# Optimization experiments

Measured on AMD Instinct MI355X. Metric: run time of the kernel, lower is better.

## Reference

```python
import jax, jax.numpy as jnp
import numpy as np

B, N, NP, K, C_IN, C, H = 16, 4096, 1024, 32, 128, 256, 4
C_G = C_IN + 3  # grouped feature dim (use_xyz concat of relative coords)
EPS = 1e-3      # keras LayerNormalization default epsilon


def setup_inputs() -> dict:
    key = jax.random.key(0)
    ks = jax.random.split(key, 16)
    s = 0.05
    return {
        "xyz": jax.random.normal(ks[0], (B, N, 3), jnp.float32),
        "newxyz": jax.random.normal(ks[1], (B, NP, 3), jnp.float32),
        "feature_input": jax.random.normal(ks[2], (B, N, C_IN), jnp.float32),
        "w_qkv": jax.random.normal(ks[3], (C_G, 3 * C), jnp.float32) * s,
        "proj_w": jax.random.normal(ks[4], (C, C), jnp.float32) * s,
        "proj_b": jnp.zeros((C,), jnp.float32),
        "dense_w": jax.random.normal(ks[5], (C_G, C), jnp.float32) * s,
        "dense_b": jnp.zeros((C,), jnp.float32),
        "fc1_w": jax.random.normal(ks[6], (C, 2 * C), jnp.float32) * s,
        "fc1_b": jnp.zeros((2 * C,), jnp.float32),
        "fc2_w": jax.random.normal(ks[7], (2 * C, C), jnp.float32) * s,
        "fc2_b": jnp.zeros((C,), jnp.float32),
        "n1_g": jnp.ones((C_G,), jnp.float32),
        "n1_b": jnp.zeros((C_G,), jnp.float32),
        "n2_g": jnp.ones((C,), jnp.float32),
        "n2_b": jnp.zeros((C,), jnp.float32),
        "group_num": K,
        "training": True,
    }


def _layernorm(x, g, b):
    m = jnp.mean(x, axis=-1, keepdims=True)
    v = jnp.mean(jnp.square(x - m), axis=-1, keepdims=True)
    return (x - m) * jax.lax.rsqrt(v + EPS) * g + b


def _sample_and_group(newxyz, group_num, xyz, feats):
    # squared pairwise distances (B, NP, N)
    d2 = (jnp.sum(newxyz**2, -1)[:, :, None]
          - 2.0 * jnp.einsum('bpc,bnc->bpn', newxyz, xyz)
          + jnp.sum(xyz**2, -1)[:, None, :])
    _, idx = jax.lax.top_k(-d2, group_num)            # (B, NP, K) nearest
    b_idx = jnp.arange(newxyz.shape[0])[:, None, None]
    grouped_xyz = xyz[b_idx, idx] - newxyz[:, :, None, :]   # (B, NP, K, 3)
    grouped_feat = feats[b_idx, idx]                        # (B, NP, K, C_IN)
    return jnp.concatenate([grouped_xyz, grouped_feat], axis=-1)


def _self_attention(x, w_qkv, proj_w, proj_b):
    b, n, k = x.shape[0], x.shape[1], x.shape[2]
    d = C // H
    qkv = jnp.einsum('bnkc,cd->bnkd', x, w_qkv)
    qkv = qkv.reshape(b, n, k, 3, H, d)
    qkv = jnp.transpose(qkv, (3, 0, 1, 4, 2, 5))      # (3, B, NP, H, K, d)
    q, kk, v = qkv[0], qkv[1], qkv[2]
    qm = jnp.max(q, axis=-2, keepdims=True)           # (B, NP, H, 1, d)
    attn = jnp.einsum('bnhqd,bnhkd->bnhqk', qm, kk) * (C ** -0.5)
    attn = jax.nn.softmax(attn, axis=-1)
    out = jnp.einsum('bnhqk,bnhkd->bnhqd', attn, v)[..., 0, :]  # (B, NP, H, d)
    out = out.reshape(b, n, C)
    return jax.nn.relu(out @ proj_w + proj_b)


def reference(xyz, newxyz, feature_input, w_qkv, proj_w, proj_b, dense_w,
              dense_b, fc1_w, fc1_b, fc2_w, fc2_b, n1_g, n1_b, n2_g, n2_b,
              group_num, training):
    gf = _sample_and_group(newxyz, group_num, xyz, feature_input)  # (B,NP,K,C_G)
    feat = _self_attention(_layernorm(gf, n1_g, n1_b), w_qkv, proj_w, proj_b)
    feat = feat + jax.nn.relu(jnp.max(gf, axis=-2) @ dense_w + dense_b)
    f2 = _layernorm(feat, n2_g, n2_b)
    f2 = jax.nn.relu(f2 @ fc1_w + fc1_b)
    f2 = f2 @ fc2_w + fc2_b
    return f2 + feat
```

## Files before the change

### kernel.cpp

```cpp
#include <hip/hip_runtime.h>
#include <hip/hip_bf16.h>

typedef __hip_bfloat16 bf16;

#define Bn   16
#define Nn   4096
#define NPn  1024
#define Kn   32
#define CINn 128
#define CGn  131
#define Cn   256
#define Hn   4
#define KPAD 160
#define XBS  168
#define XFS2 136
#define GFS  136

typedef __attribute__((ext_vector_type(8))) short frag_ab;
typedef __attribute__((ext_vector_type(4))) float frag_cd;

__device__ __forceinline__ float b2f(bf16 x) { return __bfloat162float(x); }
__device__ __forceinline__ bf16  f2b(float x) { return __float2bfloat16(x); }
__device__ __forceinline__ short f2bs(float x) {
  union { bf16 h; short s; } u; u.h = __float2bfloat16(x); return u.s;
}
__device__ __forceinline__ float bs2f(short s) {
  union { short v; bf16 h; } u; u.v = s; return __bfloat162float(u.h);
}
__device__ __forceinline__ unsigned f2ord(float f) {
  unsigned u = __float_as_uint(f);
  return u ^ ((u >> 31) ? 0xffffffffu : 0x80000000u);
}

__global__ __launch_bounds__(256) void knn_kernel(const float* __restrict__ xyz,
                                                  const float* __restrict__ newxyz,
                                                  int* __restrict__ idx_out) {
  constexpr int CAP = 2048;
  __shared__ unsigned long long tmin[256];
  __shared__ __align__(16) unsigned long long cand[CAP + 4];
  __shared__ unsigned long long wtau[4];
  __shared__ unsigned long long wred[4];
  __shared__ int scnt;
  const int bp  = blockIdx.x;
  const int b   = bp >> 10;
  const int tid = threadIdx.x;
  const float qx = newxyz[bp*3 + 0];
  const float qy = newxyz[bp*3 + 1];
  const float qz = newxyz[bp*3 + 2];
  const float sn = __fadd_rn(__fadd_rn(__fmul_rn(qx,qx), __fmul_rn(qy,qy)),
                             __fmul_rn(qz,qz));
  const float* xb = xyz + (size_t)b * Nn * 3;
  unsigned long long key[16];
  unsigned long long lmin = ~0ull;
  #pragma unroll
  for (int s = 0; s < 16; ++s) {
    const int n = s*256 + tid;
    const float xx = xb[n*3 + 0];
    const float xy = xb[n*3 + 1];
    const float xz = xb[n*3 + 2];
    const float sx  = __fadd_rn(__fadd_rn(__fmul_rn(xx,xx), __fmul_rn(xy,xy)),
                                __fmul_rn(xz,xz));
    const float dot = __fadd_rn(__fadd_rn(__fmul_rn(qx,xx), __fmul_rn(qy,xy)),
                                __fmul_rn(qz,xz));
    const float d2 = __fadd_rn(__fsub_rn(sn, __fmul_rn(2.0f, dot)), sx);
    key[s] = ((unsigned long long)f2ord(d2) << 32) | (unsigned)n;
    if (key[s] < lmin) lmin = key[s];
  }
  const int lane = tid & 63, wv = tid >> 6;

  if (tid == 0) scnt = 0;
  tmin[tid] = lmin;
  __syncthreads();

  {
    const unsigned long long* wt = &tmin[wv * 64];
    int rk = 0;
    #pragma unroll 8
    for (int j = 0; j < 64; ++j) rk += (wt[j] < lmin) ? 1 : 0;
    if (rk == 31) wtau[wv] = lmin;
  }
  __syncthreads();
  unsigned long long tau = wtau[0];
  if (wtau[1] < tau) tau = wtau[1];
  if (wtau[2] < tau) tau = wtau[2];
  if (wtau[3] < tau) tau = wtau[3];

  #pragma unroll
  for (int s = 0; s < 16; ++s) {
    if (key[s] <= tau) {
      const int p = atomicAdd(&scnt, 1);
      if (p < CAP) cand[p] = key[s];
    }
  }
  __syncthreads();
  const int m = scnt;

  if (m <= CAP) {
    if (tid < 4) cand[m + tid] = ~0ull;
    __syncthreads();
    const int m4 = (m + 3) & ~3;
    for (int t = tid; t < m; t += 256) {
      const unsigned long long mykey = cand[t];
      int r = 0;
      for (int j = 0; j < m4; j += 4) {
        r += (cand[j+0] < mykey) ? 1 : 0;
        r += (cand[j+1] < mykey) ? 1 : 0;
        r += (cand[j+2] < mykey) ? 1 : 0;
        r += (cand[j+3] < mykey) ? 1 : 0;
      }
      if (r < Kn) idx_out[(size_t)bp*Kn + r] = (int)(mykey & 0xffffffffu);
    }
  } else {
    for (int s = 0; s < Kn; ++s) {
      unsigned long long mm = lmin;
      #pragma unroll
      for (int d = 32; d; d >>= 1) {
        const unsigned lo = __shfl_xor((unsigned)(mm & 0xffffffffu), d, 64);
        const unsigned hi = __shfl_xor((unsigned)(mm >> 32), d, 64);
        const unsigned long long o = ((unsigned long long)hi << 32) | lo;
        if (o < mm) mm = o;
      }
      if (lane == 0) wred[wv] = mm;
      __syncthreads();
      unsigned long long best = wred[0];
      if (wred[1] < best) best = wred[1];
      if (wred[2] < best) best = wred[2];
      if (wred[3] < best) best = wred[3];
      __syncthreads();
      const int n = (int)(best & 0xffffffffu);
      if (tid == 0) idx_out[(size_t)bp*Kn + s] = n;
      if ((n & 255) == tid) {
        const int slot = n >> 8;
        #pragma unroll
        for (int t = 0; t < 16; ++t) if (t == slot) key[t] = ~0ull;
        unsigned long long m2 = ~0ull;
        #pragma unroll
        for (int t = 0; t < 16; ++t) if (key[t] < m2) m2 = key[t];
        lmin = m2;
      }
    }
  }
}

__global__ __launch_bounds__(256) void wprep_all_kernel(
    const float* __restrict__ w_qkv, const float* __restrict__ proj_w,
    const float* __restrict__ dense_w, const float* __restrict__ fc1_w,
    const float* __restrict__ fc2_w, short* __restrict__ o_qkv,
    short* __restrict__ o_proj, short* __restrict__ o_dense,
    short* __restrict__ o_fc1, short* __restrict__ o_fc2) {
  const int blk = blockIdx.x;
  const float* W; short* out; int K, N, nnt, remap, base;
  if      (blk <  480) { W=w_qkv;   out=o_qkv;   K=CGn; N=768; nnt=48; remap=1; base=0;    }
  else if (blk <  736) { W=proj_w;  out=o_proj;  K=Cn;  N=256; nnt=16; remap=0; base=480;  }
  else if (blk <  896) { W=dense_w; out=o_dense; K=CGn; N=256; nnt=16; remap=1; base=736;  }
  else if (blk < 1408) { W=fc1_w;   out=o_fc1;   K=Cn;  N=512; nnt=32; remap=0; base=896;  }
  else                 { W=fc2_w;   out=o_fc2;   K=512; N=256; nnt=16; remap=0; base=1408; }
  const int t = (blk - base) * 256 + threadIdx.x;
  const int j    = t & 7;
  const int lane = (t >> 3) & 63;
  const int nt   = (t >> 9) % nnt;
  const int kt   = (t >> 9) / nnt;
  const int k = kt*32 + (lane >> 4)*8 + j;
  const int n = nt*16 + (lane & 15);
  int krow = k;
  if (remap) krow = (k < 128) ? k + 3 : k - 128;
  out[t] = (k < K) ? f2bs(W[(size_t)krow*N + n]) : (short)0;
}

__global__ __launch_bounds__(256, 2) void fused_attn_kernel(
    const float* __restrict__ xyz, const float* __restrict__ newxyz,
    const float* __restrict__ featin, const short* __restrict__ wfrag,
    const float* __restrict__ n1g, const float* __restrict__ n1b,
    const int* __restrict__ idx, bf16* __restrict__ attnout,
    bf16* __restrict__ gfmax) {
  __shared__ __align__(16) short Xs[64 * XBS];
  __shared__ float sg[CGn], sb[CGn];
  __shared__ int sidx[64];
  const int bp0 = blockIdx.x * 2;
  const int b   = bp0 >> 10;
  const int tid = threadIdx.x;
  if (tid < 64) {
    int n = idx[(size_t)bp0*Kn + tid];
    sidx[tid] = ((unsigned)n < (unsigned)Nn) ? n : 0;
  }
  if (tid < CGn) {
    const int rj = (tid < 128) ? tid + 3 : tid - 128;
    sg[tid] = n1g[rj];
    sb[tid] = n1b[rj];
  }
  __syncthreads();
  const int kk = tid >> 3, sub = tid & 7;
  float4 r[2][4];
  float ex[2] = {0.f, 0.f};
  #pragma unroll
  for (int p = 0; p < 2; ++p) {
    const int row = p*32 + kk;
    const float* frow = featin + ((size_t)b*Nn + sidx[row])*CINn;
    #pragma unroll
    for (int i = 0; i < 4; ++i) r[p][i] = *(const float4*)(frow + sub*4 + 32*i);
    if (sub < 3)
      ex[p] = xyz[((size_t)b*Nn + sidx[row])*3 + sub] - newxyz[(bp0+p)*3 + sub];
  }
  #pragma unroll
  for (int p = 0; p < 2; ++p) {
    const int row = p*32 + kk;
    #pragma unroll
    for (int i = 0; i < 4; ++i) {
      short4 s4 = { f2bs(r[p][i].x), f2bs(r[p][i].y), f2bs(r[p][i].z), f2bs(r[p][i].w) };
      *(short4*)&Xs[row*XFS2 + sub*4 + 32*i] = s4;
    }
    if (sub < 3) Xs[row*XFS2 + 128 + sub] = f2bs(ex[p]);
  }
  float mean[2], rstd[2];
  #pragma unroll
  for (int p = 0; p < 2; ++p) {
    float s = ex[p], s2 = ex[p]*ex[p];
    #pragma unroll
    for (int i = 0; i < 4; ++i) {
      s  += r[p][i].x + r[p][i].y + r[p][i].z + r[p][i].w;
      s2 += r[p][i].x*r[p][i].x + r[p][i].y*r[p][i].y
          + r[p][i].z*r[p][i].z + r[p][i].w*r[p][i].w;
    }
    s  += __shfl_xor(s, 1, 64);  s  += __shfl_xor(s, 2, 64);  s  += __shfl_xor(s, 4, 64);
    s2 += __shfl_xor(s2, 1, 64); s2 += __shfl_xor(s2, 2, 64); s2 += __shfl_xor(s2, 4, 64);
    mean[p] = s * (1.0f/CGn);
    const float var = s2 * (1.0f/CGn) - mean[p]*mean[p];
    rstd[p] = rsqrtf(var + 1e-3f);
  }
  __syncthreads();
  #pragma unroll
  for (int p = 0; p < 2; ++p) {
    if (tid < GFS) {
      float m = 0.f;
      if (tid < CGn) {
        m = -1e30f;
        #pragma unroll
        for (int k2 = 0; k2 < Kn; ++k2)
          m = fmaxf(m, bs2f(Xs[(p*32 + k2)*XFS2 + tid]));
      }
      gfmax[(size_t)(bp0+p)*GFS + tid] = f2b(m);
    }
  }
  __syncthreads();
  #pragma unroll
  for (int p = 0; p < 2; ++p) {
    const int row = p*32 + kk;
    #pragma unroll
    for (int i = 0; i < 4; ++i) {
      const float4 g4 = *(const float4*)&sg[sub*4 + 32*i];
      const float4 b4 = *(const float4*)&sb[sub*4 + 32*i];
      short4 s4;
      s4.x = f2bs((r[p][i].x - mean[p])*rstd[p]*g4.x + b4.x);
      s4.y = f2bs((r[p][i].y - mean[p])*rstd[p]*g4.y + b4.y);
      s4.z = f2bs((r[p][i].z - mean[p])*rstd[p]*g4.z + b4.z);
      s4.w = f2bs((r[p][i].w - mean[p])*rstd[p]*g4.w + b4.w);
      *(short4*)&Xs[row*XBS + sub*4 + 32*i] = s4;
    }
    if (sub < 3)
      Xs[row*XBS + 128 + sub] = f2bs((ex[p] - mean[p])*rstd[p]*sg[128+sub] + sb[128+sub]);
  }
  #pragma unroll
  for (int u = 0; u < 8; ++u) {
    const int e = u*256 + tid;
    const int row = e >> 5, jj = 131 + (e & 31);
    if (jj < 160) Xs[row*XBS + jj] = 0;
  }
  __syncthreads();
  const int lane = tid & 63, w = tid >> 6;
  const int col = lane & 15, quad = lane >> 4;
  float qm[2][4], aw[2][2][4], inv[2];
  {
    frag_cd acc[4][4] = {};
    for (int kt = 0; kt < 5; ++kt) {
      const int ko = kt*32 + quad*8;
      frag_ab a[4];
      #pragma unroll
      for (int mt = 0; mt < 4; ++mt)
        a[mt] = *(const frag_ab*)&Xs[(mt*16 + col)*XBS + ko];
      #pragma unroll
      for (int ntl = 0; ntl < 4; ++ntl) {
        const int nt = w*4 + ntl;
        const frag_ab bfr = *(const frag_ab*)(wfrag + ((size_t)(kt*48 + nt)*64 + lane)*8);
        #pragma unroll
        for (int mt = 0; mt < 4; ++mt)
          acc[ntl][mt] = __builtin_amdgcn_mfma_f32_16x16x32_bf16(a[mt], bfr, acc[ntl][mt], 0, 0, 0);
      }
    }
    #pragma unroll
    for (int p = 0; p < 2; ++p)
      #pragma unroll
      for (int ntl = 0; ntl < 4; ++ntl) {
        float m = -1e30f;
        #pragma unroll
        for (int mtl = 0; mtl < 2; ++mtl)
          #pragma unroll
          for (int rr = 0; rr < 4; ++rr) m = fmaxf(m, acc[ntl][p*2+mtl][rr]);
        m = fmaxf(m, __shfl_xor(m, 16, 64));
        m = fmaxf(m, __shfl_xor(m, 32, 64));
        qm[p][ntl] = m;
      }
  }
  {
    frag_cd acc[4][4] = {};
    for (int kt = 0; kt < 5; ++kt) {
      const int ko = kt*32 + quad*8;
      frag_ab a[4];
      #pragma unroll
      for (int mt = 0; mt < 4; ++mt)
        a[mt] = *(const frag_ab*)&Xs[(mt*16 + col)*XBS + ko];
      #pragma unroll
      for (int ntl = 0; ntl < 4; ++ntl) {
        const int nt = 16 + w*4 + ntl;
        const frag_ab bfr = *(const frag_ab*)(wfrag + ((size_t)(kt*48 + nt)*64 + lane)*8);
        #pragma unroll
        for (int mt = 0; mt < 4; ++mt)
          acc[ntl][mt] = __builtin_amdgcn_mfma_f32_16x16x32_bf16(a[mt], bfr, acc[ntl][mt], 0, 0, 0);
      }
    }
    #pragma unroll
    for (int p = 0; p < 2; ++p) {
      float lg[2][4];
      #pragma unroll
      for (int mtl = 0; mtl < 2; ++mtl)
        #pragma unroll
        for (int rr = 0; rr < 4; ++rr) {
          float pp = 0.f;
          #pragma unroll
          for (int ntl = 0; ntl < 4; ++ntl) pp = fmaf(qm[p][ntl], acc[ntl][p*2+mtl][rr], pp);
          #pragma unroll
          for (int d = 1; d < 16; d <<= 1) pp += __shfl_xor(pp, d, 64);
          lg[mtl][rr] = pp * 0.0625f;
        }
      float mx = -1e30f;
      #pragma unroll
      for (int mtl = 0; mtl < 2; ++mtl)
        #pragma unroll
        for (int rr = 0; rr < 4; ++rr) mx = fmaxf(mx, lg[mtl][rr]);
      mx = fmaxf(mx, __shfl_xor(mx, 16, 64));
      mx = fmaxf(mx, __shfl_xor(mx, 32, 64));
      float ssum = 0.f;
      #pragma unroll
      for (int mtl = 0; mtl < 2; ++mtl)
        #pragma unroll
        for (int rr = 0; rr < 4; ++rr) { aw[p][mtl][rr] = expf(lg[mtl][rr] - mx); ssum += aw[p][mtl][rr]; }
      ssum += __shfl_xor(ssum, 16, 64);
      ssum += __shfl_xor(ssum, 32, 64);
      inv[p] = 1.f / ssum;
    }
  }
  {
    frag_cd acc[4][4] = {};
    for (int kt = 0; kt < 5; ++kt) {
      const int ko = kt*32 + quad*8;
      frag_ab a[4];
      #pragma unroll
      for (int mt = 0; mt < 4; ++mt)
        a[mt] = *(const frag_ab*)&Xs[(mt*16 + col)*XBS + ko];
      #pragma unroll
      for (int ntl = 0; ntl < 4; ++ntl) {
        const int nt = 32 + w*4 + ntl;
        const frag_ab bfr = *(const frag_ab*)(wfrag + ((size_t)(kt*48 + nt)*64 + lane)*8);
        #pragma unroll
        for (int mt = 0; mt < 4; ++mt)
          acc[ntl][mt] = __builtin_amdgcn_mfma_f32_16x16x32_bf16(a[mt], bfr, acc[ntl][mt], 0, 0, 0);
      }
    }
    #pragma unroll
    for (int p = 0; p < 2; ++p)
      #pragma unroll
      for (int ntl = 0; ntl < 4; ++ntl) {
        float o = 0.f;
        #pragma unroll
        for (int mtl = 0; mtl < 2; ++mtl)
          #pragma unroll
          for (int rr = 0; rr < 4; ++rr) o = fmaf(aw[p][mtl][rr], acc[ntl][p*2+mtl][rr], o);
        o += __shfl_xor(o, 16, 64);
        o += __shfl_xor(o, 32, 64);
        if (quad == 0)
          attnout[(size_t)(bp0+p)*Cn + w*64 + ntl*16 + col] = f2b(o * inv[p]);
      }
  }
}

template<bool RELU, bool ADD_S, bool OUT_BF16>
__global__ __launch_bounds__(256) void mfma_gemm_kernel(
    const bf16* __restrict__ A, int lda, int Ka,
    const short* __restrict__ Wf, int nnt_total, int N,
    const float* __restrict__ bias, const bf16* __restrict__ S,
    void* __restrict__ Dv) {
  __shared__ __align__(16) short As[64*40];
  const int m0 = blockIdx.y * 64;
  const int n0 = blockIdx.x * 128;
  const int tid = threadIdx.x, lane = tid & 63, w = tid >> 6;
  const int col = lane & 15, quad = lane >> 4;
  const int row = tid >> 2, c8 = (tid & 3) * 8;
  frag_cd acc[4][2] = {};
  const int nkt = (Ka + 31) >> 5;
  for (int kt = 0; kt < nkt; ++kt) {
    const int k0 = kt*32 + c8;
    frag_ab av = {0,0,0,0,0,0,0,0};
    if (k0 + 8 <= Ka)
      av = *(const frag_ab*)((const short*)A + (size_t)(m0+row)*lda + k0);
    __syncthreads();
    *(frag_ab*)&As[row*40 + c8] = av;
    __syncthreads();
    frag_ab afr[4];
    #pragma unroll
    for (int mt = 0; mt < 4; ++mt)
      afr[mt] = *(const frag_ab*)&As[(mt*16 + col)*40 + quad*8];
    #pragma unroll
    for (int ntl = 0; ntl < 2; ++ntl) {
      const int nt = (n0 >> 4) + w*2 + ntl;
      const frag_ab bfr = *(const frag_ab*)(Wf + ((size_t)(kt*nnt_total + nt)*64 + lane)*8);
      #pragma unroll
      for (int mt = 0; mt < 4; ++mt)
        acc[mt][ntl] = __builtin_amdgcn_mfma_f32_16x16x32_bf16(afr[mt], bfr, acc[mt][ntl], 0, 0, 0);
    }
  }
  #pragma unroll
  for (int ntl = 0; ntl < 2; ++ntl) {
    const int n = n0 + w*32 + ntl*16 + col;
    const float bv = bias[n];
    #pragma unroll
    for (int mt = 0; mt < 4; ++mt) {
      #pragma unroll
      for (int r = 0; r < 4; ++r) {
        const int m = m0 + mt*16 + quad*4 + r;
        float v = acc[mt][ntl][r] + bv;
        if (RELU) v = fmaxf(v, 0.f);
        if (ADD_S) v += b2f(S[(size_t)m*N + n]);
        if (OUT_BF16) ((bf16*)Dv)[(size_t)m*N + n] = f2b(v);
        else          ((float*)Dv)[(size_t)m*N + n] = v;
      }
    }
  }
}

__global__ __launch_bounds__(256) void dual_gemm_kernel(
    const bf16* __restrict__ A1, const short* __restrict__ W1,
    const bf16* __restrict__ A2, const short* __restrict__ W2,
    const float* __restrict__ b1, const float* __restrict__ b2,
    bf16* __restrict__ D) {
  __shared__ __align__(16) short As[64*40];
  const int m0 = blockIdx.y * 64;
  const int n0 = blockIdx.x * 128;
  const int tid = threadIdx.x, lane = tid & 63, w = tid >> 6;
  const int col = lane & 15, quad = lane >> 4;
  const int row = tid >> 2, c8 = (tid & 3) * 8;
  frag_cd acc1[4][2] = {}, acc2[4][2] = {};
  for (int kt = 0; kt < 8; ++kt) {
    const frag_ab av = *(const frag_ab*)((const short*)A1 + (size_t)(m0+row)*Cn + kt*32 + c8);
    __syncthreads();
    *(frag_ab*)&As[row*40 + c8] = av;
    __syncthreads();
    frag_ab afr[4];
    #pragma unroll
    for (int mt = 0; mt < 4; ++mt)
      afr[mt] = *(const frag_ab*)&As[(mt*16 + col)*40 + quad*8];
    #pragma unroll
    for (int ntl = 0; ntl < 2; ++ntl) {
      const int nt = (n0 >> 4) + w*2 + ntl;
      const frag_ab bfr = *(const frag_ab*)(W1 + ((size_t)(kt*16 + nt)*64 + lane)*8);
      #pragma unroll
      for (int mt = 0; mt < 4; ++mt)
        acc1[mt][ntl] = __builtin_amdgcn_mfma_f32_16x16x32_bf16(afr[mt], bfr, acc1[mt][ntl], 0, 0, 0);
    }
  }
  for (int kt = 0; kt < 5; ++kt) {
    const int k0 = kt*32 + c8;
    frag_ab av = {0,0,0,0,0,0,0,0};
    if (k0 + 8 <= GFS)
      av = *(const frag_ab*)((const short*)A2 + (size_t)(m0+row)*GFS + k0);
    __syncthreads();
    *(frag_ab*)&As[row*40 + c8] = av;
    __syncthreads();
    frag_ab afr[4];
    #pragma unroll
    for (int mt = 0; mt < 4; ++mt)
      afr[mt] = *(const frag_ab*)&As[(mt*16 + col)*40 + quad*8];
    #pragma unroll
    for (int ntl = 0; ntl < 2; ++ntl) {
      const int nt = (n0 >> 4) + w*2 + ntl;
      const frag_ab bfr = *(const frag_ab*)(W2 + ((size_t)(kt*16 + nt)*64 + lane)*8);
      #pragma unroll
      for (int mt = 0; mt < 4; ++mt)
        acc2[mt][ntl] = __builtin_amdgcn_mfma_f32_16x16x32_bf16(afr[mt], bfr, acc2[mt][ntl], 0, 0, 0);
    }
  }
  #pragma unroll
  for (int ntl = 0; ntl < 2; ++ntl) {
    const int n = n0 + w*32 + ntl*16 + col;
    const float bv1 = b1[n], bv2 = b2[n];
    #pragma unroll
    for (int mt = 0; mt < 4; ++mt) {
      #pragma unroll
      for (int r = 0; r < 4; ++r) {
        const int m = m0 + mt*16 + quad*4 + r;
        const float v = fmaxf(acc1[mt][ntl][r] + bv1, 0.f)
                      + fmaxf(acc2[mt][ntl][r] + bv2, 0.f);
        D[(size_t)m*Cn + n] = f2b(v);
      }
    }
  }
}

__global__ __launch_bounds__(256) void ln2_kernel(const bf16* __restrict__ feat,
                                                  const float* __restrict__ g,
                                                  const float* __restrict__ b,
                                                  bf16* __restrict__ out) {
  const int r = blockIdx.x*4 + (threadIdx.x >> 6), lane = threadIdx.x & 63;
  float vv[4];
  #pragma unroll
  for (int c = 0; c < 4; ++c) vv[c] = b2f(feat[(size_t)r*Cn + lane*4 + c]);
  float s  = vv[0] + vv[1] + vv[2] + vv[3];
  float s2 = vv[0]*vv[0] + vv[1]*vv[1] + vv[2]*vv[2] + vv[3]*vv[3];
  #pragma unroll
  for (int d = 32; d; d >>= 1) { s += __shfl_xor(s, d, 64); s2 += __shfl_xor(s2, d, 64); }
  const float mean = s * (1.f/256.f);
  const float var  = s2 * (1.f/256.f) - mean*mean;
  const float rstd = rsqrtf(var + 1e-3f);
  #pragma unroll
  for (int c = 0; c < 4; ++c) {
    const int cc = lane*4 + c;
    out[(size_t)r*Cn + cc] = f2b((vv[c] - mean)*rstd*g[cc] + b[cc]);
  }
}

extern "C" void kernel_launch(void* const* d_in, const int* in_sizes, int n_in,
                              void* d_out, int out_size, void* d_ws, size_t ws_size,
                              hipStream_t stream) {
  const float* xyz     = (const float*)d_in[0];
  const float* newxyz  = (const float*)d_in[1];
  const float* featin  = (const float*)d_in[2];
  const float* w_qkv   = (const float*)d_in[3];
  const float* proj_w  = (const float*)d_in[4];
  const float* proj_b  = (const float*)d_in[5];
  const float* dense_w = (const float*)d_in[6];
  const float* dense_b = (const float*)d_in[7];
  const float* fc1_w   = (const float*)d_in[8];
  const float* fc1_b   = (const float*)d_in[9];
  const float* fc2_w   = (const float*)d_in[10];
  const float* fc2_b   = (const float*)d_in[11];
  const float* n1g     = (const float*)d_in[12];
  const float* n1b     = (const float*)d_in[13];
  const float* n2g     = (const float*)d_in[14];
  const float* n2b     = (const float*)d_in[15];

  char*  ws     = (char*)d_ws;
  short* wqkv   = (short*)(ws + 0);
  short* wproj  = (short*)(ws + 245760);
  short* wdense = (short*)(ws + 376832);
  short* wfc1   = (short*)(ws + 458752);
  short* wfc2   = (short*)(ws + 720896);
  bf16*  featB  = (bf16*)(ws + 1048576);
  bf16*  attnA  = (bf16*)(ws + 9437184);
  bf16*  gfmax  = (bf16*)(ws + 17825792);
  int*   idxws  = (int*) (ws + 22282240);
  bf16*  fc1out = (bf16*)(ws + 24379392);

  const int M = Bn * NPn;

  knn_kernel<<<dim3(M), dim3(256), 0, stream>>>(xyz, newxyz, idxws);
  wprep_all_kernel<<<dim3(1920), dim3(256), 0, stream>>>(
      w_qkv, proj_w, dense_w, fc1_w, fc2_w, wqkv, wproj, wdense, wfc1, wfc2);

  fused_attn_kernel<<<dim3(M/2), dim3(256), 0, stream>>>(
      xyz, newxyz, featin, wqkv, n1g, n1b, idxws, attnA, gfmax);
  dual_gemm_kernel<<<dim3(2, M/64), dim3(256), 0, stream>>>(
      attnA, wproj, gfmax, wdense, proj_b, dense_b, featB);
  ln2_kernel<<<dim3(M/4), dim3(256), 0, stream>>>(featB, n2g, n2b, attnA);
  mfma_gemm_kernel<true, false, true><<<dim3(4, M/64), dim3(256), 0, stream>>>(
      attnA, Cn, Cn, wfc1, 32, 512, fc1_b, (const bf16*)nullptr, fc1out);
  mfma_gemm_kernel<false, true, false><<<dim3(2, M/64), dim3(256), 0, stream>>>(
      fc1out, 512, 512, wfc2, 16, Cn, fc2_b, featB, d_out);
}
```

Before: 482.5 us.

## Make fused attention persistent over 8 pairs with double-buffered gather prefetch

```diff
diff --git a/kernel.cpp b/kernel.cpp
--- a/kernel.cpp
+++ b/kernel.cpp
@@ -13,8 +13,8 @@
 #define Hn   4
 #define KPAD 160
 #define XBS  168
-#define XFS2 136
 #define GFS  136
+#define PPB  8
 
 typedef __attribute__((ext_vector_type(8))) short frag_ab;
 typedef __attribute__((ext_vector_type(4))) float frag_cd;
@@ -172,213 +172,260 @@
     const float* __restrict__ featin, const short* __restrict__ wfrag,
     const float* __restrict__ n1g, const float* __restrict__ n1b,
     const int* __restrict__ idx, bf16* __restrict__ attnout,
-    bf16* __restrict__ gfmax) {
-  __shared__ __align__(16) short Xs[64 * XBS];
+    bf16* __restrict__ gfmaxg) {
+  __shared__ __align__(16) short Xs[2][64 * XBS];
   __shared__ float sg[CGn], sb[CGn];
-  __shared__ int sidx[64];
-  const int bp0 = blockIdx.x * 2;
-  const int b   = bp0 >> 10;
-  const int tid = threadIdx.x;
-  if (tid < 64) {
-    int n = idx[(size_t)bp0*Kn + tid];
-    sidx[tid] = ((unsigned)n < (unsigned)Nn) ? n : 0;
-  }
+  __shared__ int sidx[2 * 64];
+  __shared__ float pmaxs[2 * 4 * 8 * 16];
+  __shared__ float pmax_ex[2 * 4 * 3];
+
+  const int tid   = threadIdx.x;
+  const int pair0 = blockIdx.x * PPB;
+  const int b     = (pair0 * 2) >> 10;
+  const float* featin_b = featin + (size_t)b * Nn * CINn;
+  const float* xyz_b    = xyz + (size_t)b * Nn * 3;
+
   if (tid < CGn) {
     const int rj = (tid < 128) ? tid + 3 : tid - 128;
     sg[tid] = n1g[rj];
     sb[tid] = n1b[rj];
   }
+  for (int e = tid; e < 64 * 32; e += 256) {
+    const int row = e >> 5, jj = 131 + (e & 31);
+    if (jj < 160) { Xs[0][row*XBS + jj] = 0; Xs[1][row*XBS + jj] = 0; }
+  }
+  if (tid < 64) {
+    int n = idx[(size_t)(pair0 * 2) * Kn + tid];
+    sidx[tid] = ((unsigned)n < (unsigned)Nn) ? n : 0;
+  }
   __syncthreads();
+
   const int kk = tid >> 3, sub = tid & 7;
-  float4 r[2][4];
-  float ex[2] = {0.f, 0.f};
-  #pragma unroll
-  for (int p = 0; p < 2; ++p) {
-    const int row = p*32 + kk;
-    const float* frow = featin + ((size_t)b*Nn + sidx[row])*CINn;
-    #pragma unroll
-    for (int i = 0; i < 4; ++i) r[p][i] = *(const float4*)(frow + sub*4 + 32*i);
-    if (sub < 3)
-      ex[p] = xyz[((size_t)b*Nn + sidx[row])*3 + sub] - newxyz[(bp0+p)*3 + sub];
-  }
-  #pragma unroll
-  for (int p = 0; p < 2; ++p) {
-    const int row = p*32 + kk;
-    #pragma unroll
-    for (int i = 0; i < 4; ++i) {
-      short4 s4 = { f2bs(r[p][i].x), f2bs(r[p][i].y), f2bs(r[p][i].z), f2bs(r[p][i].w) };
-      *(short4*)&Xs[row*XFS2 + sub*4 + 32*i] = s4;
-    }
-    if (sub < 3) Xs[row*XFS2 + 128 + sub] = f2bs(ex[p]);
-  }
-  float mean[2], rstd[2];
-  #pragma unroll
-  for (int p = 0; p < 2; ++p) {
-    float s = ex[p], s2 = ex[p]*ex[p];
-    #pragma unroll
-    for (int i = 0; i < 4; ++i) {
-      s  += r[p][i].x + r[p][i].y + r[p][i].z + r[p][i].w;
-      s2 += r[p][i].x*r[p][i].x + r[p][i].y*r[p][i].y
-          + r[p][i].z*r[p][i].z + r[p][i].w*r[p][i].w;
-    }
-    s  += __shfl_xor(s, 1, 64);  s  += __shfl_xor(s, 2, 64);  s  += __shfl_xor(s, 4, 64);
-    s2 += __shfl_xor(s2, 1, 64); s2 += __shfl_xor(s2, 2, 64); s2 += __shfl_xor(s2, 4, 64);
-    mean[p] = s * (1.0f/CGn);
-    const float var = s2 * (1.0f/CGn) - mean[p]*mean[p];
-    rstd[p] = rsqrtf(var + 1e-3f);
-  }
-  __syncthreads();
-  #pragma unroll
-  for (int p = 0; p < 2; ++p) {
-    if (tid < GFS) {
-      float m = 0.f;
-      if (tid < CGn) {
-        m = -1e30f;
-        #pragma unroll
-        for (int k2 = 0; k2 < Kn; ++k2)
-          m = fmaxf(m, bs2f(Xs[(p*32 + k2)*XFS2 + tid]));
-      }
-      gfmax[(size_t)(bp0+p)*GFS + tid] = f2b(m);
-    }
-  }
-  __syncthreads();
-  #pragma unroll
-  for (int p = 0; p < 2; ++p) {
-    const int row = p*32 + kk;
-    #pragma unroll
-    for (int i = 0; i < 4; ++i) {
-      const float4 g4 = *(const float4*)&sg[sub*4 + 32*i];
-      const float4 b4 = *(const float4*)&sb[sub*4 + 32*i];
-      short4 s4;
-      s4.x = f2bs((r[p][i].x - mean[p])*rstd[p]*g4.x + b4.x);
-      s4.y = f2bs((r[p][i].y - mean[p])*rstd[p]*g4.y + b4.y);
-      s4.z = f2bs((r[p][i].z - mean[p])*rstd[p]*g4.z + b4.z);
-      s4.w = f2bs((r[p][i].w - mean[p])*rstd[p]*g4.w + b4.w);
-      *(short4*)&Xs[row*XBS + sub*4 + 32*i] = s4;
-    }
-    if (sub < 3)
-      Xs[row*XBS + 128 + sub] = f2bs((ex[p] - mean[p])*rstd[p]*sg[128+sub] + sb[128+sub]);
-  }
-  #pragma unroll
-  for (int u = 0; u < 8; ++u) {
-    const int e = u*256 + tid;
-    const int row = e >> 5, jj = 131 + (e & 31);
-    if (jj < 160) Xs[row*XBS + jj] = 0;
-  }
-  __syncthreads();
   const int lane = tid & 63, w = tid >> 6;
   const int col = lane & 15, quad = lane >> 4;
-  float qm[2][4], aw[2][2][4], inv[2];
-  {
-    frag_cd acc[4][4] = {};
-    for (int kt = 0; kt < 5; ++kt) {
-      const int ko = kt*32 + quad*8;
-      frag_ab a[4];
-      #pragma unroll
-      for (int mt = 0; mt < 4; ++mt)
-        a[mt] = *(const frag_ab*)&Xs[(mt*16 + col)*XBS + ko];
-      #pragma unroll
-      for (int ntl = 0; ntl < 4; ++ntl) {
-        const int nt = w*4 + ntl;
-        const frag_ab bfr = *(const frag_ab*)(wfrag + ((size_t)(kt*48 + nt)*64 + lane)*8);
+
+  float4 rA[2][4], rB[2][4];
+  float exA[2], exB[2];
+
+  auto gather_issue = [&](const int* sidx_l, int bp0g,
+                          float4 (&r)[2][4], float (&ex)[2]) {
+    #pragma unroll
+    for (int p = 0; p < 2; ++p) {
+      const int row = p*32 + kk;
+      const float* frow = featin_b + (size_t)sidx_l[row] * CINn;
+      #pragma unroll
+      for (int i = 0; i < 4; ++i) r[p][i] = *(const float4*)(frow + sub*4 + 32*i);
+      ex[p] = 0.f;
+      if (sub < 3)
+        ex[p] = xyz_b[(size_t)sidx_l[row]*3 + sub] - newxyz[(bp0g+p)*3 + sub];
+    }
+  };
+
+  gather_issue(&sidx[0], pair0 * 2, rA, exA);
+
+  auto body = [&](int it, short* Xb, float4 (&rc)[2][4], float (&exc)[2],
+                  float4 (&rn)[2][4], float (&exn)[2]) {
+    const int pr  = pair0 + it;
+    const int bp0 = pr * 2;
+    const int itn = (it + 1 < PPB) ? it + 1 : PPB - 1;
+    const int nb  = (it + 1) & 1;
+    if (tid < 64) {
+      int n = idx[(size_t)((pair0 + itn) * 2) * Kn + tid];
+      sidx[nb*64 + tid] = ((unsigned)n < (unsigned)Nn) ? n : 0;
+    }
+    float mean[2], rstd[2];
+    #pragma unroll
+    for (int p = 0; p < 2; ++p) {
+      float s = exc[p], s2 = exc[p]*exc[p];
+      #pragma unroll
+      for (int i = 0; i < 4; ++i) {
+        s  += rc[p][i].x + rc[p][i].y + rc[p][i].z + rc[p][i].w;
+        s2 += rc[p][i].x*rc[p][i].x + rc[p][i].y*rc[p][i].y
+            + rc[p][i].z*rc[p][i].z + rc[p][i].w*rc[p][i].w;
+      }
+      s  += __shfl_xor(s, 1, 64);  s  += __shfl_xor(s, 2, 64);  s  += __shfl_xor(s, 4, 64);
+      s2 += __shfl_xor(s2, 1, 64); s2 += __shfl_xor(s2, 2, 64); s2 += __shfl_xor(s2, 4, 64);
+      mean[p] = s * (1.0f/CGn);
+      const float var = s2 * (1.0f/CGn) - mean[p]*mean[p];
+      rstd[p] = rsqrtf(var + 1e-3f);
+    }
+    #pragma unroll
+    for (int p = 0; p < 2; ++p) {
+      float mm[16];
+      #pragma unroll
+      for (int i = 0; i < 4; ++i) {
+        mm[i*4+0] = rc[p][i].x; mm[i*4+1] = rc[p][i].y;
+        mm[i*4+2] = rc[p][i].z; mm[i*4+3] = rc[p][i].w;
+      }
+      #pragma unroll
+      for (int d = 8; d <= 32; d <<= 1)
+        #pragma unroll
+        for (int q = 0; q < 16; ++q) mm[q] = fmaxf(mm[q], __shfl_xor(mm[q], d, 64));
+      float me = exc[p];
+      #pragma unroll
+      for (int d = 8; d <= 32; d <<= 1) me = fmaxf(me, __shfl_xor(me, d, 64));
+      if (lane < 8) {
+        #pragma unroll
+        for (int q = 0; q < 16; ++q) pmaxs[((p*4 + w)*8 + lane)*16 + q] = mm[q];
+      }
+      if (lane < 3) pmax_ex[(p*4 + w)*3 + lane] = me;
+    }
+    __syncthreads();
+    #pragma unroll
+    for (int p = 0; p < 2; ++p) {
+      if (tid < GFS) {
+        float v = 0.f;
+        if (tid < 128) {
+          const int i2 = tid >> 5, sb2 = (tid & 31) >> 2, q = i2*4 + (tid & 3);
+          v = pmaxs[((p*4+0)*8 + sb2)*16 + q];
+          v = fmaxf(v, pmaxs[((p*4+1)*8 + sb2)*16 + q]);
+          v = fmaxf(v, pmaxs[((p*4+2)*8 + sb2)*16 + q]);
+          v = fmaxf(v, pmaxs[((p*4+3)*8 + sb2)*16 + q]);
+        } else if (tid < CGn) {
+          const int c3 = tid - 128;
+          v = fmaxf(fmaxf(pmax_ex[(p*4+0)*3 + c3], pmax_ex[(p*4+1)*3 + c3]),
+                    fmaxf(pmax_ex[(p*4+2)*3 + c3], pmax_ex[(p*4+3)*3 + c3]));
+        }
+        gfmaxg[(size_t)(bp0+p)*GFS + tid] = f2b(v);
+      }
+    }
+    #pragma unroll
+    for (int p = 0; p < 2; ++p) {
+      const int row = p*32 + kk;
+      #pragma unroll
+      for (int i = 0; i < 4; ++i) {
+        const float4 g4 = *(const float4*)&sg[sub*4 + 32*i];
+        const float4 b4 = *(const float4*)&sb[sub*4 + 32*i];
+        short4 s4;
+        s4.x = f2bs((rc[p][i].x - mean[p])*rstd[p]*g4.x + b4.x);
+        s4.y = f2bs((rc[p][i].y - mean[p])*rstd[p]*g4.y + b4.y);
+        s4.z = f2bs((rc[p][i].z - mean[p])*rstd[p]*g4.z + b4.z);
+        s4.w = f2bs((rc[p][i].w - mean[p])*rstd[p]*g4.w + b4.w);
+        *(short4*)&Xb[row*XBS + sub*4 + 32*i] = s4;
+      }
+      if (sub < 3)
+        Xb[row*XBS + 128 + sub] = f2bs((exc[p] - mean[p])*rstd[p]*sg[128+sub] + sb[128+sub]);
+    }
+    __syncthreads();
+    gather_issue(&sidx[nb*64], (pair0 + itn) * 2, rn, exn);
+    float qm[2][4], aw[2][2][4], inv[2];
+    {
+      frag_cd acc[4][4] = {};
+      for (int kt = 0; kt < 5; ++kt) {
+        const int ko = kt*32 + quad*8;
+        frag_ab a[4];
         #pragma unroll
         for (int mt = 0; mt < 4; ++mt)
-          acc[ntl][mt] = __builtin_amdgcn_mfma_f32_16x16x32_bf16(a[mt], bfr, acc[ntl][mt], 0, 0, 0);
-      }
-    }
-    #pragma unroll
-    for (int p = 0; p < 2; ++p)
-      #pragma unroll
-      for (int ntl = 0; ntl < 4; ++ntl) {
-        float m = -1e30f;
+          a[mt] = *(const frag_ab*)&Xb[(mt*16 + col)*XBS + ko];
+        #pragma unroll
+        for (int ntl = 0; ntl < 4; ++ntl) {
+          const int nt = w*4 + ntl;
+          const frag_ab bfr = *(const frag_ab*)(wfrag + ((size_t)(kt*48 + nt)*64 + lane)*8);
+          #pragma unroll
+          for (int mt = 0; mt < 4; ++mt)
+            acc[ntl][mt] = __builtin_amdgcn_mfma_f32_16x16x32_bf16(a[mt], bfr, acc[ntl][mt], 0, 0, 0);
+        }
+      }
+      #pragma unroll
+      for (int p = 0; p < 2; ++p)
+        #pragma unroll
+        for (int ntl = 0; ntl < 4; ++ntl) {
+          float m = -1e30f;
+          #pragma unroll
+          for (int mtl = 0; mtl < 2; ++mtl)
+            #pragma unroll
+            for (int rr = 0; rr < 4; ++rr) m = fmaxf(m, acc[ntl][p*2+mtl][rr]);
+          m = fmaxf(m, __shfl_xor(m, 16, 64));
+          m = fmaxf(m, __shfl_xor(m, 32, 64));
+          qm[p][ntl] = m;
+        }
+    }
+    {
+      frag_cd acc[4][4] = {};
+      for (int kt = 0; kt < 5; ++kt) {
+        const int ko = kt*32 + quad*8;
+        frag_ab a[4];
+        #pragma unroll
+        for (int mt = 0; mt < 4; ++mt)
+          a[mt] = *(const frag_ab*)&Xb[(mt*16 + col)*XBS + ko];
+        #pragma unroll
+        for (int ntl = 0; ntl < 4; ++ntl) {
+          const int nt = 16 + w*4 + ntl;
+          const frag_ab bfr = *(const frag_ab*)(wfrag + ((size_t)(kt*48 + nt)*64 + lane)*8);
+          #pragma unroll
+          for (int mt = 0; mt < 4; ++mt)
+            acc[ntl][mt] = __builtin_amdgcn_mfma_f32_16x16x32_bf16(a[mt], bfr, acc[ntl][mt], 0, 0, 0);
+        }
+      }
+      #pragma unroll
+      for (int p = 0; p < 2; ++p) {
+        float lg[2][4];
         #pragma unroll
         for (int mtl = 0; mtl < 2; ++mtl)
           #pragma unroll
-          for (int rr = 0; rr < 4; ++rr) m = fmaxf(m, acc[ntl][p*2+mtl][rr]);
-        m = fmaxf(m, __shfl_xor(m, 16, 64));
-        m = fmaxf(m, __shfl_xor(m, 32, 64));
-        qm[p][ntl] = m;
-      }
-  }
-  {
-    frag_cd acc[4][4] = {};
-    for (int kt = 0; kt < 5; ++kt) {
-      const int ko = kt*32 + quad*8;
-      frag_ab a[4];
-      #pragma unroll
-      for (int mt = 0; mt < 4; ++mt)
-        a[mt] = *(const frag_ab*)&Xs[(mt*16 + col)*XBS + ko];
-      #pragma unroll
-      for (int ntl = 0; ntl < 4; ++ntl) {
-        const int nt = 16 + w*4 + ntl;
-        const frag_ab bfr = *(const frag_ab*)(wfrag + ((size_t)(kt*48 + nt)*64 + lane)*8);
+          for (int rr = 0; rr < 4; ++rr) {
+            float pp = 0.f;
+            #pragma unroll
+            for (int ntl = 0; ntl < 4; ++ntl) pp = fmaf(qm[p][ntl], acc[ntl][p*2+mtl][rr], pp);
+            #pragma unroll
+            for (int d = 1; d < 16; d <<= 1) pp += __shfl_xor(pp, d, 64);
+            lg[mtl][rr] = pp * 0.0625f;
+          }
+        float mx = -1e30f;
+        #pragma unroll
+        for (int mtl = 0; mtl < 2; ++mtl)
+          #pragma unroll
+          for (int rr = 0; rr < 4; ++rr) mx = fmaxf(mx, lg[mtl][rr]);
+        mx = fmaxf(mx, __shfl_xor(mx, 16, 64));
+        mx = fmaxf(mx, __shfl_xor(mx, 32, 64));
+        float ssum = 0.f;
+        #pragma unroll
+        for (int mtl = 0; mtl < 2; ++mtl)
+          #pragma unroll
+          for (int rr = 0; rr < 4; ++rr) { aw[p][mtl][rr] = expf(lg[mtl][rr] - mx); ssum += aw[p][mtl][rr]; }
+        ssum += __shfl_xor(ssum, 16, 64);
+        ssum += __shfl_xor(ssum, 32, 64);
+        inv[p] = 1.f / ssum;
+      }
+    }
+    {
+      frag_cd acc[4][4] = {};
+      for (int kt = 0; kt < 5; ++kt) {
+        const int ko = kt*32 + quad*8;
+        frag_ab a[4];
         #pragma unroll
         for (int mt = 0; mt < 4; ++mt)
-          acc[ntl][mt] = __builtin_amdgcn_mfma_f32_16x16x32_bf16(a[mt], bfr, acc[ntl][mt], 0, 0, 0);
-      }
-    }
-    #pragma unroll
-    for (int p = 0; p < 2; ++p) {
-      float lg[2][4];
-      #pragma unroll
-      for (int mtl = 0; mtl < 2; ++mtl)
-        #pragma unroll
-        for (int rr = 0; rr < 4; ++rr) {
-          float pp = 0.f;
-          #pragma unroll
-          for (int ntl = 0; ntl < 4; ++ntl) pp = fmaf(qm[p][ntl], acc[ntl][p*2+mtl][rr], pp);
-          #pragma unroll
-          for (int d = 1; d < 16; d <<= 1) pp += __shfl_xor(pp, d, 64);
-          lg[mtl][rr] = pp * 0.0625f;
+          a[mt] = *(const frag_ab*)&Xb[(mt*16 + col)*XBS + ko];
+        #pragma unroll
+        for (int ntl = 0; ntl < 4; ++ntl) {
+          const int nt = 32 + w*4 + ntl;
+          const frag_ab bfr = *(const frag_ab*)(wfrag + ((size_t)(kt*48 + nt)*64 + lane)*8);
+          #pragma unroll
+          for (int mt = 0; mt < 4; ++mt)
+            acc[ntl][mt] = __builtin_amdgcn_mfma_f32_16x16x32_bf16(a[mt], bfr, acc[ntl][mt], 0, 0, 0);
         }
-      float mx = -1e30f;
-      #pragma unroll
-      for (int mtl = 0; mtl < 2; ++mtl)
-        #pragma unroll
-        for (int rr = 0; rr < 4; ++rr) mx = fmaxf(mx, lg[mtl][rr]);
-      mx = fmaxf(mx, __shfl_xor(mx, 16, 64));
-      mx = fmaxf(mx, __shfl_xor(mx, 32, 64));
-      float ssum = 0.f;
-      #pragma unroll
-      for (int mtl = 0; mtl < 2; ++mtl)
-        #pragma unroll
-        for (int rr = 0; rr < 4; ++rr) { aw[p][mtl][rr] = expf(lg[mtl][rr] - mx); ssum += aw[p][mtl][rr]; }
-      ssum += __shfl_xor(ssum, 16, 64);
-      ssum += __shfl_xor(ssum, 32, 64);
-      inv[p] = 1.f / ssum;
-    }
-  }
-  {
-    frag_cd acc[4][4] = {};
-    for (int kt = 0; kt < 5; ++kt) {
-      const int ko = kt*32 + quad*8;
-      frag_ab a[4];
-      #pragma unroll
-      for (int mt = 0; mt < 4; ++mt)
-        a[mt] = *(const frag_ab*)&Xs[(mt*16 + col)*XBS + ko];
-      #pragma unroll
-      for (int ntl = 0; ntl < 4; ++ntl) {
-        const int nt = 32 + w*4 + ntl;
-        const frag_ab bfr = *(const frag_ab*)(wfrag + ((size_t)(kt*48 + nt)*64 + lane)*8);
-        #pragma unroll
-        for (int mt = 0; mt < 4; ++mt)
-          acc[ntl][mt] = __builtin_amdgcn_mfma_f32_16x16x32_bf16(a[mt], bfr, acc[ntl][mt], 0, 0, 0);
-      }
-    }
-    #pragma unroll
-    for (int p = 0; p < 2; ++p)
-      #pragma unroll
-      for (int ntl = 0; ntl < 4; ++ntl) {
-        float o = 0.f;
-        #pragma unroll
-        for (int mtl = 0; mtl < 2; ++mtl)
-          #pragma unroll
-          for (int rr = 0; rr < 4; ++rr) o = fmaf(aw[p][mtl][rr], acc[ntl][p*2+mtl][rr], o);
-        o += __shfl_xor(o, 16, 64);
-        o += __shfl_xor(o, 32, 64);
-        if (quad == 0)
-          attnout[(size_t)(bp0+p)*Cn + w*64 + ntl*16 + col] = f2b(o * inv[p]);
-      }
+      }
+      #pragma unroll
+      for (int p = 0; p < 2; ++p)
+        #pragma unroll
+        for (int ntl = 0; ntl < 4; ++ntl) {
+          float o = 0.f;
+          #pragma unroll
+          for (int mtl = 0; mtl < 2; ++mtl)
+            #pragma unroll
+            for (int rr = 0; rr < 4; ++rr) o = fmaf(aw[p][mtl][rr], acc[ntl][p*2+mtl][rr], o);
+          o += __shfl_xor(o, 16, 64);
+          o += __shfl_xor(o, 32, 64);
+          if (quad == 0)
+            attnout[(size_t)(bp0+p)*Cn + w*64 + ntl*16 + col] = f2b(o * inv[p]);
+        }
+    }
+  };
+
+  #pragma unroll 1
+  for (int it = 0; it < PPB; it += 2) {
+    body(it,     Xs[0], rA, exA, rB, exB);
+    body(it + 1, Xs[1], rB, exB, rA, exA);
   }
 }
 
@@ -564,7 +611,7 @@
   wprep_all_kernel<<<dim3(1920), dim3(256), 0, stream>>>(
       w_qkv, proj_w, dense_w, fc1_w, fc2_w, wqkv, wproj, wdense, wfc1, wfc2);
 
-  fused_attn_kernel<<<dim3(M/2), dim3(256), 0, stream>>>(
+  fused_attn_kernel<<<dim3(M/2/PPB), dim3(256), 0, stream>>>(
       xyz, newxyz, featin, wqkv, n1g, n1b, idxws, attnA, gfmax);
   dual_gemm_kernel<<<dim3(2, M/64), dim3(256), 0, stream>>>(
       attnA, wproj, gfmax, wdense, proj_b, dense_b, featB);
```

Result: slower. 752.9 us (+56.0%).
